# Performance work log

Measured on AMD Instinct MI355X. Metric: run time of the kernel, lower is better.

Reference implementation:

```python
import jax, jax.numpy as jnp
import numpy as np

D = 2048      # d_model
H = 32        # n_heads
DS = 64       # d_state = d_model // n_heads
K = 4         # conv kernel size (hardcoded in module)
EPS = 1e-6


def setup_inputs() -> dict:
    key = jax.random.key(0)
    ks = jax.random.split(key, 8)
    B, L = 2, 4096
    s = lambda k, shp, sc: jax.random.normal(k, shp, dtype=jnp.float32) * sc
    return {
        "x": s(ks[0], (B, L, D), 1.0),
        "state": jnp.zeros((B, H, DS), jnp.float32),
        "norm_w": jnp.ones((D,), jnp.float32),
        "conv_w": s(ks[1], (D, K), 0.5),          # depthwise conv weight [d_model, K]
        "conv_b": s(ks[2], (D,), 0.1),
        "pp_w": s(ks[3], (D, 3 * H * DS), 0.02),  # param_proj (stored [in, out])
        "pp_b": jnp.zeros((3 * H * DS,), jnp.float32),
        "gp_w": s(ks[4], (D, D), 0.02),           # gate_proj
        "gp_b": jnp.zeros((D,), jnp.float32),
        "op_w": s(ks[5], (D, D), 0.02),           # out_proj
        "op_b": jnp.zeros((D,), jnp.float32),
    }


def reference(x, state, norm_w, conv_w, conv_b, pp_w, pp_b, gp_w, gp_b, op_w, op_b):
    B, L, Dm = x.shape
    # RMSNorm
    rms = jnp.sqrt(jnp.mean(x * x, axis=-1, keepdims=True) + EPS)
    xn = norm_w * x / rms
    # causal depthwise conv1d + SiLU (pad left K-1, valid cross-correlation)
    xp = jnp.pad(xn, ((0, 0), (K - 1, 0), (0, 0)))
    xc = conv_b + sum(xp[:, k:k + L, :] * conv_w[:, k] for k in range(K))
    xc = jax.nn.silu(xc)
    gate = jax.nn.sigmoid(xc @ gp_w + gp_b)                  # [B, L, D]
    p = (xn @ pp_w + pp_b).reshape(B, L, H, 3, DS)
    delta = jax.nn.sigmoid(p[..., 0, :])                     # [B, L, H, DS]
    Bm, Cm = p[..., 1, :], p[..., 2, :]
    # sequential recurrence h_t = delta_t * h_{t-1} + B_t, time-major scan
    dt = jnp.moveaxis(delta, 1, 0)                           # [L, B, H, DS]
    Bt = jnp.moveaxis(Bm, 1, 0)
    def step(h, db):
        d, b = db
        h = d * h + b
        return h, h
    h_last, hs = jax.lax.scan(step, state, (dt, Bt))         # hs: [L, B, H, DS]
    ssm = (jnp.moveaxis(Cm, 1, 0) * hs).reshape(L, B, Dm)
    ssm = jnp.moveaxis(ssm, 0, 1)                            # [B, L, D]
    mixed = gate * ssm + (1.0 - gate) * xn
    y = mixed @ op_w + op_b + x
    return y, h_last
```

## Files before the change

### kernel.cpp

```cpp
#include <hip/hip_runtime.h>
#include <math.h>

#define BB   2
#define LL   4096
#define DD   2048
#define HH   32
#define DSS  64
#define MM   (BB * LL)
#define N3   (3 * HH * DSS)
#define NCH  64
#define CLN  64
#define EPSF 1e-6f
#define GP_NB (DD / 128)
#define PP_NB (N3 / 128)

typedef unsigned short bf16;
typedef __attribute__((ext_vector_type(8))) short bf16x8;
typedef __attribute__((ext_vector_type(4))) float f32x4;

__device__ __forceinline__ float bf2f(bf16 u) {
    union { unsigned int i; float f; } v;
    v.i = ((unsigned int)u) << 16;
    return v.f;
}
__device__ __forceinline__ bf16 f2bf(float f) {
    union { float f; unsigned int u; } v;
    v.f = f;
    unsigned int r = (v.u >> 16) & 1u;
    return (bf16)((v.u + 0x7fffu + r) >> 16);
}
__device__ __forceinline__ float sigmoidf_(float v) {
    return 1.0f / (1.0f + __expf(-v));
}
__device__ __forceinline__ void gload16(const void* g, void* l) {
    __builtin_amdgcn_global_load_lds(
        (const __attribute__((address_space(1))) void*)g,
        (__attribute__((address_space(3))) void*)l, 16, 0, 0);
}

__global__ __launch_bounds__(256) void rms_kernel(const float* __restrict__ x,
                                                  const float* __restrict__ w,
                                                  bf16* __restrict__ xn) {
    int row = blockIdx.x;
    const float4* x4 = (const float4*)(x + (size_t)row * DD);
    ushort4* o4 = (ushort4*)(xn + (size_t)row * DD);
    const float4* w4 = (const float4*)w;
    int t = threadIdx.x;
    float4 v0 = x4[t], v1 = x4[t + 256];
    float ss = v0.x * v0.x + v0.y * v0.y + v0.z * v0.z + v0.w * v0.w +
               v1.x * v1.x + v1.y * v1.y + v1.z * v1.z + v1.w * v1.w;
#pragma unroll
    for (int off = 32; off >= 1; off >>= 1) ss += __shfl_down(ss, off, 64);
    __shared__ float red[4];
    if ((t & 63) == 0) red[t >> 6] = ss;
    __syncthreads();
    float tot = red[0] + red[1] + red[2] + red[3];
    float inv = 1.0f / sqrtf(tot * (1.0f / DD) + EPSF);
    float4 wa = w4[t], wb = w4[t + 256];
    ushort4 r0, r1;
    r0.x = f2bf(v0.x * inv * wa.x); r0.y = f2bf(v0.y * inv * wa.y);
    r0.z = f2bf(v0.z * inv * wa.z); r0.w = f2bf(v0.w * inv * wa.w);
    r1.x = f2bf(v1.x * inv * wb.x); r1.y = f2bf(v1.y * inv * wb.y);
    r1.z = f2bf(v1.z * inv * wb.z); r1.w = f2bf(v1.w * inv * wb.w);
    o4[t] = r0; o4[t + 256] = r1;
}

#define CONV_LC 32
__global__ __launch_bounds__(256) void conv_silu_kernel(const bf16* __restrict__ xn,
                                                        const float* __restrict__ cw,
                                                        const float* __restrict__ cb,
                                                        bf16* __restrict__ xc) {
    int b = blockIdx.z;
    int l0 = blockIdx.x * CONV_LC;
    int d0 = blockIdx.y * 1024 + threadIdx.x * 4;
    float4 w[4];
    float bias[4];
#pragma unroll
    for (int j = 0; j < 4; ++j) {
        w[j] = ((const float4*)cw)[d0 + j];
        bias[j] = cb[d0 + j];
    }
    float win[3][4];
#pragma unroll
    for (int k = 0; k < 3; ++k) {
        int l = l0 - 3 + k;
        if (l >= 0) {
            ushort4 v = *(const ushort4*)&xn[((size_t)b * LL + l) * DD + d0];
            win[k][0] = bf2f(v.x); win[k][1] = bf2f(v.y);
            win[k][2] = bf2f(v.z); win[k][3] = bf2f(v.w);
        } else {
            win[k][0] = win[k][1] = win[k][2] = win[k][3] = 0.0f;
        }
    }
    size_t off = ((size_t)b * LL + l0) * DD + d0;
    for (int i = 0; i < CONV_LC; ++i) {
        ushort4 v = *(const ushort4*)&xn[off];
        float cur[4] = {bf2f(v.x), bf2f(v.y), bf2f(v.z), bf2f(v.w)};
        ushort4 o;
#pragma unroll
        for (int j = 0; j < 4; ++j) {
            float acc = bias[j] + win[0][j] * w[j].x + win[1][j] * w[j].y +
                        win[2][j] * w[j].z + cur[j] * w[j].w;
            float s = acc * sigmoidf_(acc);
            ((unsigned short*)&o)[j] = f2bf(s);
        }
        *(ushort4*)&xc[off] = o;
#pragma unroll
        for (int j = 0; j < 4; ++j) {
            win[0][j] = win[1][j]; win[1][j] = win[2][j]; win[2][j] = cur[j];
        }
        off += DD;
    }
}

__global__ __launch_bounds__(256) void transpose3(const float* __restrict__ gp_w,
                                                  const float* __restrict__ op_w,
                                                  const float* __restrict__ pp_w,
                                                  bf16* __restrict__ gp_wT,
                                                  bf16* __restrict__ op_wT,
                                                  bf16* __restrict__ pp_wT) {
    __shared__ float t[32][33];
    int bx = blockIdx.x;
    const float* W; bf16* WT; int Ndim;
    if (bx < 64)       { W = gp_w; WT = gp_wT; Ndim = DD; }
    else if (bx < 128) { W = op_w; WT = op_wT; Ndim = DD; bx -= 64; }
    else               { W = pp_w; WT = pp_wT; Ndim = N3; bx -= 128; }
    int n0 = bx << 5, k0 = blockIdx.y << 5;
    int tx = threadIdx.x & 31;
    int ty = threadIdx.x >> 5;
#pragma unroll
    for (int i = 0; i < 32; i += 8)
        t[ty + i][tx] = W[(size_t)(k0 + ty + i) * Ndim + n0 + tx];
    __syncthreads();
#pragma unroll
    for (int i = 0; i < 32; i += 8)
        WT[(size_t)(n0 + ty + i) * DD + k0 + tx] = f2bf(t[tx][ty + i]);
}

template <int EPI, typename OutT>
__device__ __forceinline__ void gemm_tile(const bf16* __restrict__ A,
                                          const bf16* __restrict__ Bt,
                                          const float* __restrict__ bias,
                                          const float* __restrict__ add,
                                          OutT* __restrict__ out,
                                          int Ndim, int m0, int n0,
                                          bf16* As, bf16* Bs) {
    const int tid  = threadIdx.x;
    const int wave = tid >> 6;
    const int lane = tid & 63;
    const int sr = lane >> 3;
    const int gcol = ((lane & 7) ^ sr) << 3;
    const bf16* gA[4];
    const bf16* gB[4];
    bf16* lA[4];
    bf16* lB[4];
#pragma unroll
    for (int p = 0; p < 4; ++p) {
        int c = wave * 4 + p;
        gA[p] = A  + (size_t)(m0 + c * 8 + sr) * DD + gcol;
        gB[p] = Bt + (size_t)(n0 + c * 8 + sr) * DD + gcol;
        lA[p] = As + c * 512 + lane * 8;
        lB[p] = Bs + c * 512 + lane * 8;
    }
    const int wm = (wave >> 1) << 6;
    const int wn = (wave & 1) << 6;
    const int fr = lane & 15;
    const int kg = lane >> 4;
    const int f7 = fr & 7;

    f32x4 acc[4][4] = {};
    for (int k0 = 0; k0 < DD; k0 += 64) {
        __syncthreads();
#pragma unroll
        for (int p = 0; p < 4; ++p) {
            gload16(gA[p] + k0, lA[p]);
            gload16(gB[p] + k0, lB[p]);
        }
        __syncthreads();
#pragma unroll
        for (int ks = 0; ks < 2; ++ks) {
            bf16x8 af[4], bf_[4];
#pragma unroll
            for (int i = 0; i < 4; ++i) {
                int gq = (((ks << 2) | kg) ^ f7) << 3;
                af[i]  = *(const bf16x8*)&As[(wm + i * 16 + fr) * 64 + gq];
                bf_[i] = *(const bf16x8*)&Bs[(wn + i * 16 + fr) * 64 + gq];
            }
#pragma unroll
            for (int i = 0; i < 4; ++i)
#pragma unroll
                for (int j = 0; j < 4; ++j)
                    acc[i][j] = __builtin_amdgcn_mfma_f32_16x16x32_bf16(
                        af[i], bf_[j], acc[i][j], 0, 0, 0);
        }
    }
    const int baseRow = m0 + wm + kg * 4;
    const int baseCol = n0 + wn + fr;
#pragma unroll
    for (int i = 0; i < 4; ++i) {
#pragma unroll
        for (int r = 0; r < 4; ++r) {
            int m = baseRow + i * 16 + r;
            size_t rowoff = (size_t)m * Ndim + baseCol;
#pragma unroll
            for (int j = 0; j < 4; ++j) {
                float v = acc[i][j][r] + bias[baseCol + j * 16];
                if (EPI == 1) v = sigmoidf_(v);
                if (EPI == 2) v += add[rowoff + j * 16];
                if constexpr (sizeof(OutT) == 4)
                    ((float*)out)[rowoff + j * 16] = v;
                else
                    ((bf16*)out)[rowoff + j * 16] = f2bf(v);
            }
        }
    }
}

__global__ __launch_bounds__(256) void gemm_gateproj(const bf16* __restrict__ xc,
                                                     const bf16* __restrict__ gp_wT,
                                                     const float* __restrict__ gp_b,
                                                     bf16* __restrict__ gate,
                                                     const bf16* __restrict__ xn,
                                                     const bf16* __restrict__ pp_wT,
                                                     const float* __restrict__ pp_b,
                                                     bf16* __restrict__ p) {
    __shared__ __align__(16) bf16 As[128 * 64];
    __shared__ __align__(16) bf16 Bs[128 * 64];
    const int m0 = blockIdx.y << 7;
    if (blockIdx.x < GP_NB) {
        gemm_tile<1, bf16>(xc, gp_wT, gp_b, nullptr, gate, DD,
                           m0, blockIdx.x << 7, As, Bs);
    } else {
        gemm_tile<0, bf16>(xn, pp_wT, pp_b, nullptr, p, N3,
                           m0, (blockIdx.x - GP_NB) << 7, As, Bs);
    }
}

__global__ __launch_bounds__(256) void gemm_out(const bf16* __restrict__ mixed,
                                                const bf16* __restrict__ op_wT,
                                                const float* __restrict__ op_b,
                                                const float* __restrict__ x,
                                                float* __restrict__ y) {
    __shared__ __align__(16) bf16 As[128 * 64];
    __shared__ __align__(16) bf16 Bs[128 * 64];
    gemm_tile<2, float>(mixed, op_wT, op_b, x, y, DD,
                        blockIdx.y << 7, blockIdx.x << 7, As, Bs);
}

__global__ __launch_bounds__(256) void scan_phase1(const bf16* __restrict__ p,
                                                   float* __restrict__ cA,
                                                   float* __restrict__ cB) {
    int c = blockIdx.x, b = blockIdx.z, s = threadIdx.x & 63;
    int h = blockIdx.y * 4 + (threadIdx.x >> 6);
    size_t base = ((size_t)(b * LL + c * CLN)) * N3 + h * (3 * DSS) + s;
    float a = 1.0f, bb = 0.0f;
    for (int i = 0; i < CLN; ++i) {
        float d = sigmoidf_(bf2f(p[base]));
        float Bv = bf2f(p[base + DSS]);
        a *= d;
        bb = d * bb + Bv;
        base += N3;
    }
    int idx = ((b * HH + h) * NCH + c) * DSS + s;
    cA[idx] = a;
    cB[idx] = bb;
}

__global__ __launch_bounds__(64) void scan_phase2(const float* __restrict__ state,
                                                  const float* __restrict__ cA,
                                                  const float* __restrict__ cB,
                                                  float* __restrict__ cH,
                                                  float* __restrict__ hlast) {
    int h = blockIdx.x, b = blockIdx.y, s = threadIdx.x;
    float hp = state[(b * HH + h) * DSS + s];
    int base = ((b * HH + h) * NCH) * DSS + s;
    for (int c = 0; c < NCH; ++c) {
        cH[base + c * DSS] = hp;
        hp = cA[base + c * DSS] * hp + cB[base + c * DSS];
    }
    hlast[(b * HH + h) * DSS + s] = hp;
}

__global__ __launch_bounds__(256) void scan_phase3(const bf16* __restrict__ p,
                                                   const float* __restrict__ cH,
                                                   const bf16* __restrict__ gate,
                                                   const bf16* __restrict__ xn,
                                                   bf16* __restrict__ mixed) {
    int c = blockIdx.x, b = blockIdx.z, s = threadIdx.x & 63;
    int h = blockIdx.y * 4 + (threadIdx.x >> 6);
    float hp = cH[((b * HH + h) * NCH + c) * DSS + s];
    size_t prow = ((size_t)(b * LL + c * CLN)) * N3 + h * (3 * DSS) + s;
    size_t grow = ((size_t)(b * LL + c * CLN)) * DD + h * DSS + s;
    for (int i = 0; i < CLN; ++i) {
        float d = sigmoidf_(bf2f(p[prow]));
        float Bv = bf2f(p[prow + DSS]);
        float Cv = bf2f(p[prow + 2 * DSS]);
        hp = d * hp + Bv;
        float ssm = Cv * hp;
        float g = bf2f(gate[grow]);
        float xv = bf2f(xn[grow]);
        mixed[grow] = f2bf(g * ssm + (1.0f - g) * xv);
        prow += N3;
        grow += DD;
    }
}

extern "C" void kernel_launch(void* const* d_in, const int* in_sizes, int n_in,
                              void* d_out, int out_size, void* d_ws, size_t ws_size,
                              hipStream_t stream) {
    const float* x      = (const float*)d_in[0];
    const float* state  = (const float*)d_in[1];
    const float* norm_w = (const float*)d_in[2];
    const float* conv_w = (const float*)d_in[3];
    const float* conv_b = (const float*)d_in[4];
    const float* pp_w   = (const float*)d_in[5];
    const float* pp_b   = (const float*)d_in[6];
    const float* gp_w   = (const float*)d_in[7];
    const float* gp_b   = (const float*)d_in[8];
    const float* op_w   = (const float*)d_in[9];
    const float* op_b   = (const float*)d_in[10];

    float* y     = (float*)d_out;
    float* hlast = y + (size_t)MM * DD;

    const size_t BHND = (size_t)BB * HH * NCH * DSS;
    char* ws = (char*)d_ws;
    bf16* xn    = (bf16*)ws;
    bf16* xcbuf = xn + (size_t)MM * DD;
    bf16* p     = xcbuf + (size_t)MM * DD;
    float* cA   = (float*)(p + (size_t)MM * N3);
    float* cB   = cA + BHND;
    float* cH   = cB + BHND;
    bf16* gp_wT = (bf16*)(cH + BHND);
    bf16* op_wT = gp_wT + (size_t)DD * DD;
    bf16* gate  = (bf16*)y;
    bf16* pp_wT = gate + (size_t)MM * DD;
    bf16* mixed = xcbuf;

    rms_kernel<<<MM, 256, 0, stream>>>(x, norm_w, xn);
    conv_silu_kernel<<<dim3(LL / CONV_LC, DD / 1024, BB), 256, 0, stream>>>(
        xn, conv_w, conv_b, xcbuf);
    transpose3<<<dim3(320, DD / 32), 256, 0, stream>>>(gp_w, op_w, pp_w,
                                                       gp_wT, op_wT, pp_wT);
    gemm_gateproj<<<dim3(GP_NB + PP_NB, MM / 128), 256, 0, stream>>>(
        xcbuf, gp_wT, gp_b, gate, xn, pp_wT, pp_b, p);
    scan_phase1<<<dim3(NCH, HH / 4, BB), 256, 0, stream>>>(p, cA, cB);
    scan_phase2<<<dim3(HH, BB), 64, 0, stream>>>(state, cA, cB, cH, hlast);
    scan_phase3<<<dim3(NCH, HH / 4, BB), 256, 0, stream>>>(p, cH, gate, xn, mixed);
    gemm_out<<<dim3(GP_NB, MM / 128), 256, 0, stream>>>(mixed, op_wT, op_b, x, y);
}
```

Baseline: 682.5 us.

## Fuse RMSNorm with weight transpose and fold scan phase2 into phase3

Merges the RMSNorm and weight-transpose kernels into one launch, with the transpose now writing bf16 pairs. It also removes the serial scan_phase2 kernel by having each phase3 block recompute its starting state from the chunk carries. Separately, it halves the conv chunk length and adds unroll pragmas to the conv and scan loops. Together these cut two launches and a tiny serial kernel. The cost is redundant prefix work in phase3, up to 63 carry steps per block.

```diff
diff --git a/kernel.cpp b/kernel.cpp
--- a/kernel.cpp
+++ b/kernel.cpp
@@ -13,6 +13,8 @@
 #define EPSF 1e-6f
 #define GP_NB (DD / 128)
 #define PP_NB (N3 / 128)
+#define TR_NBX 320
+#define TR_NBY (DD / 32)
 
 typedef unsigned short bf16;
 typedef __attribute__((ext_vector_type(8))) short bf16x8;
@@ -38,34 +40,64 @@
         (__attribute__((address_space(3))) void*)l, 16, 0, 0);
 }
 
-__global__ __launch_bounds__(256) void rms_kernel(const float* __restrict__ x,
-                                                  const float* __restrict__ w,
-                                                  bf16* __restrict__ xn) {
-    int row = blockIdx.x;
-    const float4* x4 = (const float4*)(x + (size_t)row * DD);
-    ushort4* o4 = (ushort4*)(xn + (size_t)row * DD);
-    const float4* w4 = (const float4*)w;
+__global__ __launch_bounds__(256) void rms_transpose(const float* __restrict__ x,
+                                                     const float* __restrict__ w,
+                                                     bf16* __restrict__ xn,
+                                                     const float* __restrict__ gp_w,
+                                                     const float* __restrict__ op_w,
+                                                     const float* __restrict__ pp_w,
+                                                     bf16* __restrict__ gp_wT,
+                                                     bf16* __restrict__ op_wT,
+                                                     bf16* __restrict__ pp_wT) {
+    __shared__ float sh[32 * 33];
     int t = threadIdx.x;
-    float4 v0 = x4[t], v1 = x4[t + 256];
-    float ss = v0.x * v0.x + v0.y * v0.y + v0.z * v0.z + v0.w * v0.w +
-               v1.x * v1.x + v1.y * v1.y + v1.z * v1.z + v1.w * v1.w;
-#pragma unroll
-    for (int off = 32; off >= 1; off >>= 1) ss += __shfl_down(ss, off, 64);
-    __shared__ float red[4];
-    if ((t & 63) == 0) red[t >> 6] = ss;
-    __syncthreads();
-    float tot = red[0] + red[1] + red[2] + red[3];
-    float inv = 1.0f / sqrtf(tot * (1.0f / DD) + EPSF);
-    float4 wa = w4[t], wb = w4[t + 256];
-    ushort4 r0, r1;
-    r0.x = f2bf(v0.x * inv * wa.x); r0.y = f2bf(v0.y * inv * wa.y);
-    r0.z = f2bf(v0.z * inv * wa.z); r0.w = f2bf(v0.w * inv * wa.w);
-    r1.x = f2bf(v1.x * inv * wb.x); r1.y = f2bf(v1.y * inv * wb.y);
-    r1.z = f2bf(v1.z * inv * wb.z); r1.w = f2bf(v1.w * inv * wb.w);
-    o4[t] = r0; o4[t + 256] = r1;
-}
-
-#define CONV_LC 32
+    if (blockIdx.x < MM) {
+        int row = blockIdx.x;
+        const float4* x4 = (const float4*)(x + (size_t)row * DD);
+        ushort4* o4 = (ushort4*)(xn + (size_t)row * DD);
+        const float4* w4 = (const float4*)w;
+        float4 v0 = x4[t], v1 = x4[t + 256];
+        float ss = v0.x * v0.x + v0.y * v0.y + v0.z * v0.z + v0.w * v0.w +
+                   v1.x * v1.x + v1.y * v1.y + v1.z * v1.z + v1.w * v1.w;
+#pragma unroll
+        for (int off = 32; off >= 1; off >>= 1) ss += __shfl_down(ss, off, 64);
+        if ((t & 63) == 0) sh[t >> 6] = ss;
+        __syncthreads();
+        float tot = sh[0] + sh[1] + sh[2] + sh[3];
+        float inv = 1.0f / sqrtf(tot * (1.0f / DD) + EPSF);
+        float4 wa = w4[t], wb = w4[t + 256];
+        ushort4 r0, r1;
+        r0.x = f2bf(v0.x * inv * wa.x); r0.y = f2bf(v0.y * inv * wa.y);
+        r0.z = f2bf(v0.z * inv * wa.z); r0.w = f2bf(v0.w * inv * wa.w);
+        r1.x = f2bf(v1.x * inv * wb.x); r1.y = f2bf(v1.y * inv * wb.y);
+        r1.z = f2bf(v1.z * inv * wb.z); r1.w = f2bf(v1.w * inv * wb.w);
+        o4[t] = r0; o4[t + 256] = r1;
+    } else {
+        int id = blockIdx.x - MM;
+        int bx = id % TR_NBX;
+        int k0 = (id / TR_NBX) << 5;
+        const float* W; bf16* WT; int Ndim;
+        if (bx < 64)       { W = gp_w; WT = gp_wT; Ndim = DD; }
+        else if (bx < 128) { W = op_w; WT = op_wT; Ndim = DD; bx -= 64; }
+        else               { W = pp_w; WT = pp_wT; Ndim = N3; bx -= 128; }
+        int n0 = bx << 5;
+        float (*tl)[33] = (float (*)[33])sh;
+        int tx = t & 31, ty = t >> 5;
+#pragma unroll
+        for (int i = 0; i < 32; i += 8)
+            tl[ty + i][tx] = W[(size_t)(k0 + ty + i) * Ndim + n0 + tx];
+        __syncthreads();
+        int tx2 = t & 15, ty2 = t >> 4;
+#pragma unroll
+        for (int i = 0; i < 32; i += 16) {
+            int n = ty2 + i;
+            ushort2 v = { f2bf(tl[tx2 * 2][n]), f2bf(tl[tx2 * 2 + 1][n]) };
+            *(ushort2*)&WT[(size_t)(n0 + n) * DD + k0 + tx2 * 2] = v;
+        }
+    }
+}
+
+#define CONV_LC 16
 __global__ __launch_bounds__(256) void conv_silu_kernel(const bf16* __restrict__ xn,
                                                         const float* __restrict__ cw,
                                                         const float* __restrict__ cb,
@@ -93,6 +125,7 @@
         }
     }
     size_t off = ((size_t)b * LL + l0) * DD + d0;
+#pragma unroll 4
     for (int i = 0; i < CONV_LC; ++i) {
         ushort4 v = *(const ushort4*)&xn[off];
         float cur[4] = {bf2f(v.x), bf2f(v.y), bf2f(v.z), bf2f(v.w)};
@@ -111,30 +144,6 @@
         }
         off += DD;
     }
-}
-
-__global__ __launch_bounds__(256) void transpose3(const float* __restrict__ gp_w,
-                                                  const float* __restrict__ op_w,
-                                                  const float* __restrict__ pp_w,
-                                                  bf16* __restrict__ gp_wT,
-                                                  bf16* __restrict__ op_wT,
-                                                  bf16* __restrict__ pp_wT) {
-    __shared__ float t[32][33];
-    int bx = blockIdx.x;
-    const float* W; bf16* WT; int Ndim;
-    if (bx < 64)       { W = gp_w; WT = gp_wT; Ndim = DD; }
-    else if (bx < 128) { W = op_w; WT = op_wT; Ndim = DD; bx -= 64; }
-    else               { W = pp_w; WT = pp_wT; Ndim = N3; bx -= 128; }
-    int n0 = bx << 5, k0 = blockIdx.y << 5;
-    int tx = threadIdx.x & 31;
-    int ty = threadIdx.x >> 5;
-#pragma unroll
-    for (int i = 0; i < 32; i += 8)
-        t[ty + i][tx] = W[(size_t)(k0 + ty + i) * Ndim + n0 + tx];
-    __syncthreads();
-#pragma unroll
-    for (int i = 0; i < 32; i += 8)
-        WT[(size_t)(n0 + ty + i) * DD + k0 + tx] = f2bf(t[tx][ty + i]);
 }
 
 template <int EPI, typename OutT>
@@ -247,6 +256,7 @@
                         blockIdx.y << 7, blockIdx.x << 7, As, Bs);
 }
 
+
 __global__ __launch_bounds__(256) void scan_phase1(const bf16* __restrict__ p,
                                                    float* __restrict__ cA,
                                                    float* __restrict__ cB) {
@@ -254,6 +264,7 @@
     int h = blockIdx.y * 4 + (threadIdx.x >> 6);
     size_t base = ((size_t)(b * LL + c * CLN)) * N3 + h * (3 * DSS) + s;
     float a = 1.0f, bb = 0.0f;
+#pragma unroll 8
     for (int i = 0; i < CLN; ++i) {
         float d = sigmoidf_(bf2f(p[base]));
         float Bv = bf2f(p[base + DSS]);
@@ -266,31 +277,23 @@
     cB[idx] = bb;
 }
 
-__global__ __launch_bounds__(64) void scan_phase2(const float* __restrict__ state,
-                                                  const float* __restrict__ cA,
-                                                  const float* __restrict__ cB,
-                                                  float* __restrict__ cH,
-                                                  float* __restrict__ hlast) {
-    int h = blockIdx.x, b = blockIdx.y, s = threadIdx.x;
-    float hp = state[(b * HH + h) * DSS + s];
-    int base = ((b * HH + h) * NCH) * DSS + s;
-    for (int c = 0; c < NCH; ++c) {
-        cH[base + c * DSS] = hp;
-        hp = cA[base + c * DSS] * hp + cB[base + c * DSS];
-    }
-    hlast[(b * HH + h) * DSS + s] = hp;
-}
-
 __global__ __launch_bounds__(256) void scan_phase3(const bf16* __restrict__ p,
-                                                   const float* __restrict__ cH,
+                                                   const float* __restrict__ cA,
+                                                   const float* __restrict__ cB,
+                                                   const float* __restrict__ state,
                                                    const bf16* __restrict__ gate,
                                                    const bf16* __restrict__ xn,
-                                                   bf16* __restrict__ mixed) {
+                                                   bf16* __restrict__ mixed,
+                                                   float* __restrict__ hlast) {
     int c = blockIdx.x, b = blockIdx.z, s = threadIdx.x & 63;
     int h = blockIdx.y * 4 + (threadIdx.x >> 6);
-    float hp = cH[((b * HH + h) * NCH + c) * DSS + s];
+    float hp = state[(b * HH + h) * DSS + s];
+    int cbase = ((b * HH + h) * NCH) * DSS + s;
+    for (int cc = 0; cc < c; ++cc)
+        hp = cA[cbase + cc * DSS] * hp + cB[cbase + cc * DSS];
     size_t prow = ((size_t)(b * LL + c * CLN)) * N3 + h * (3 * DSS) + s;
     size_t grow = ((size_t)(b * LL + c * CLN)) * DD + h * DSS + s;
+#pragma unroll 4
     for (int i = 0; i < CLN; ++i) {
         float d = sigmoidf_(bf2f(p[prow]));
         float Bv = bf2f(p[prow + DSS]);
@@ -303,6 +306,7 @@
         prow += N3;
         grow += DD;
     }
+    if (c == NCH - 1) hlast[(b * HH + h) * DSS + s] = hp;
 }
 
 extern "C" void kernel_launch(void* const* d_in, const int* in_sizes, int n_in,
@@ -330,22 +334,20 @@
     bf16* p     = xcbuf + (size_t)MM * DD;
     float* cA   = (float*)(p + (size_t)MM * N3);
     float* cB   = cA + BHND;
-    float* cH   = cB + BHND;
-    bf16* gp_wT = (bf16*)(cH + BHND);
+    bf16* gp_wT = (bf16*)(cB + BHND);
     bf16* op_wT = gp_wT + (size_t)DD * DD;
     bf16* gate  = (bf16*)y;
     bf16* pp_wT = gate + (size_t)MM * DD;
     bf16* mixed = xcbuf;
 
-    rms_kernel<<<MM, 256, 0, stream>>>(x, norm_w, xn);
+    rms_transpose<<<MM + TR_NBX * TR_NBY, 256, 0, stream>>>(
+        x, norm_w, xn, gp_w, op_w, pp_w, gp_wT, op_wT, pp_wT);
     conv_silu_kernel<<<dim3(LL / CONV_LC, DD / 1024, BB), 256, 0, stream>>>(
         xn, conv_w, conv_b, xcbuf);
-    transpose3<<<dim3(320, DD / 32), 256, 0, stream>>>(gp_w, op_w, pp_w,
-                                                       gp_wT, op_wT, pp_wT);
     gemm_gateproj<<<dim3(GP_NB + PP_NB, MM / 128), 256, 0, stream>>>(
         xcbuf, gp_wT, gp_b, gate, xn, pp_wT, pp_b, p);
     scan_phase1<<<dim3(NCH, HH / 4, BB), 256, 0, stream>>>(p, cA, cB);
-    scan_phase2<<<dim3(HH, BB), 64, 0, stream>>>(state, cA, cB, cH, hlast);
-    scan_phase3<<<dim3(NCH, HH / 4, BB), 256, 0, stream>>>(p, cH, gate, xn, mixed);
+    scan_phase3<<<dim3(NCH, HH / 4, BB), 256, 0, stream>>>(
+        p, cA, cB, state, gate, xn, mixed, hlast);
     gemm_out<<<dim3(GP_NB, MM / 128), 256, 0, stream>>>(mixed, op_wT, op_b, x, y);
 }
```

New measurement: 666.4 us. 1.02x faster.
